# Optimization experiments

Measured on AMD Instinct MI355X. Metric: run time of the kernel, lower is better.

The kernel has to match this reference:

```python
import jax, jax.numpy as jnp
from jax import lax
import numpy as np

SEQ, BATCH, X_DIM = 256, 64, 64
FEAT = 256      # dense_x[-1]
DEC = 256       # dense_h_x[-1]
H = 512         # dim_rnn


def setup_inputs() -> dict:
    key = jax.random.key(0)
    ks = jax.random.split(key, 12)
    s = 0.05
    return {
        "x": jax.random.normal(ks[0], (SEQ, BATCH, X_DIM), jnp.float32),
        "mode_selector": jax.random.uniform(ks[1], (SEQ,), jnp.float32),
        # feature extractor: Linear(x_dim -> FEAT) + tanh
        "W_fx": jax.random.normal(ks[2], (FEAT, X_DIM), jnp.float32) * s,
        "b_fx": jnp.zeros((FEAT,), jnp.float32),
        # LSTM (single layer): gates ordered i, f, g, o (torch convention)
        "W_ih": jax.random.normal(ks[3], (4 * H, FEAT), jnp.float32) * s,
        "W_hh": jax.random.normal(ks[4], (4 * H, H), jnp.float32) * s,
        "b_ih": jnp.zeros((4 * H,), jnp.float32),
        "b_hh": jnp.zeros((4 * H,), jnp.float32),
        # decoder MLP: Linear(H -> DEC) + tanh
        "W_hx": jax.random.normal(ks[5], (DEC, H), jnp.float32) * s,
        "b_hx": jnp.zeros((DEC,), jnp.float32),
        # gen_out: Linear(DEC -> x_dim)
        "W_out": jax.random.normal(ks[6], (X_DIM, DEC), jnp.float32) * s,
        "b_out": jnp.zeros((X_DIM,), jnp.float32),
    }


def _forward(x, mode_selector, W_fx, b_fx, W_ih, W_hh, b_ih, b_hh,
             W_hx, b_hx, W_out, b_out):
    def fe(v):  # feature_extractor_x (dropout_p=0 -> identity)
        return jnp.tanh(v @ W_fx.T + b_fx)

    def gen(h):  # mlp_h_x + gen_out
        return jnp.tanh(h @ W_hx.T + b_hx) @ W_out.T + b_out

    def lstm_cell(feat, h, c):
        g = feat @ W_ih.T + b_ih + h @ W_hh.T + b_hh  # [B, 4H]
        i, f, gg, o = jnp.split(g, 4, axis=-1)
        c2 = jax.nn.sigmoid(f) * c + jax.nn.sigmoid(i) * jnp.tanh(gg)
        h2 = jax.nn.sigmoid(o) * jnp.tanh(c2)
        return h2, c2

    S, B, _ = x.shape
    feat_x = fe(x)  # [S, B, FEAT] teacher-forced features
    h0 = jnp.zeros((B, H), x.dtype)
    c0 = jnp.zeros((B, H), x.dtype)
    y0 = jnp.zeros((B, W_out.shape[0]), x.dtype)

    def step(carry, inp):
        h, c, y_prev = carry
        feat_tf, mix, is_first = inp
        # at t=0 original uses feature_x[0] as the "auto" feature
        feat_auto = jnp.where(is_first, feat_tf, fe(y_prev))
        feat = mix * feat_auto + (1.0 - mix) * feat_tf
        y_t = gen(h)           # generated from pre-update hidden state
        h2, c2 = lstm_cell(feat, h, c)
        return (h2, c2, y_t), y_t

    is_first = (jnp.arange(S) == 0)
    _, y = lax.scan(step, (h0, c0, y0), (feat_x, mode_selector, is_first))
    return y  # [S, B, x_dim]


def reference(x, mode_selector, W_fx, b_fx, W_ih, W_hh, b_ih, b_hh,
              W_hx, b_hx, W_out, b_out):
    return _forward(x, mode_selector, W_fx, b_fx, W_ih, W_hh, b_ih, b_hh,
                    W_hx, b_hx, W_out, b_out)
```

## Files before the change

kernel.cpp:

```cpp
#include <hip/hip_runtime.h>
#include <stdint.h>

typedef unsigned short u16;
typedef unsigned int u32;
typedef unsigned long long u64;
typedef __attribute__((ext_vector_type(8))) short short8;
typedef __attribute__((ext_vector_type(4))) float f32x4;
typedef __attribute__((ext_vector_type(4))) int int4v;

#define SEQ 256
#define GATE_WGS 64
#define D_WGS 8
#define NWG 73
#define A_ELE 49152
#define D_ELE 16384

__device__ __forceinline__ u16 f2bf(float f) {
  u32 u = __float_as_uint(f);
  u += 0x7FFFu + ((u >> 16) & 1u);
  return (u16)(u >> 16);
}
__device__ __forceinline__ float bf2f(u16 v) {
  return __uint_as_float(((u32)v) << 16);
}
__device__ __forceinline__ short8 cvt8(const float* __restrict__ p) {
  short8 r;
#pragma unroll
  for (int j = 0; j < 8; ++j) r[j] = (short)f2bf(p[j]);
  return r;
}
__device__ __forceinline__ short8 cvt8v(const float* __restrict__ p) {
  f32x4 a = *(const f32x4*)p, b = *(const f32x4*)(p + 4);
  short8 r;
#pragma unroll
  for (int j = 0; j < 4; ++j) { r[j] = (short)f2bf(a[j]); r[4 + j] = (short)f2bf(b[j]); }
  return r;
}
__device__ __forceinline__ float fast_tanh(float x) {
  return 1.0f - 2.0f / (1.0f + __expf(2.0f * x));
}
__device__ __forceinline__ float fast_sig(float x) {
  return 1.0f / (1.0f + __expf(-x));
}

union V16 { short8 s; u64 q[2]; };
__device__ __forceinline__ short8 ldc16(const u16* p) {
  V16 v;
  v.q[0] = __hip_atomic_load((const u64*)p,     __ATOMIC_RELAXED, __HIP_MEMORY_SCOPE_AGENT);
  v.q[1] = __hip_atomic_load((const u64*)p + 1, __ATOMIC_RELAXED, __HIP_MEMORY_SCOPE_AGENT);
  return v.s;
}
__device__ __forceinline__ void stc16(u16* p, const u64* s) {
  __hip_atomic_store((u64*)p,     s[0], __ATOMIC_RELAXED, __HIP_MEMORY_SCOPE_AGENT);
  __hip_atomic_store((u64*)p + 1, s[1], __ATOMIC_RELAXED, __HIP_MEMORY_SCOPE_AGENT);
}
__device__ __forceinline__ void pollge(u32* p, u32 v) {
  while (__hip_atomic_load(p, __ATOMIC_RELAXED, __HIP_MEMORY_SCOPE_AGENT) < v) {}
}
__device__ __forceinline__ void setflag(u32* p, u32 v) {
  __hip_atomic_store(p, v, __ATOMIC_RELAXED, __HIP_MEMORY_SCOPE_AGENT);
}
#define VMCNT0() asm volatile("s_waitcnt vmcnt(0)" ::: "memory")

__global__ void prep_misc(const float* __restrict__ W_fx, const float* __restrict__ b_fx,
                          const float* __restrict__ W_out, const float* __restrict__ b_out,
                          u16* __restrict__ Abuf0, u32* __restrict__ flags,
                          float* __restrict__ bcomb, u16* __restrict__ Wcpack) {
  int b = blockIdx.x, tid = threadIdx.x;
  if (b == 0) {
    for (int it = 0; it < 16; ++it) {
      int chunk = it * 256 + tid;
      *(int4v*)(Abuf0 + (2048 + chunk) * 8) = (int4v){0, 0, 0, 0};
    }
  } else if (b == 1) {
    for (int k = 0; k < 6; ++k) flags[k * 256 + tid] = 0u;
  } else if (b == 2) {
    float s = b_fx[tid];
    for (int k = 0; k < 64; ++k) s += W_fx[tid * 64 + k] * b_out[k];
    bcomb[tid] = s;
  } else {
    int ct = b - 3;
    for (int it = 0; it < 16; ++it) {
      int o = it * 256 + tid;
      int cl = o >> 8, dec = o & 255;
      int c = ct * 16 + cl;
      float s = 0.f;
      for (int k = 0; k < 64; ++k) s += W_fx[c * 64 + k] * W_out[k * 256 + dec];
      int dwk = dec >> 5, kd = dec & 31;
      int l = (c & 15) + ((kd >> 3) << 4), j = kd & 7;
      Wcpack[((dwk * 16 + (c >> 4)) * 64 + l) * 8 + j] = f2bf(s);
    }
  }
}

__global__ void prep_ftf(const float* __restrict__ x, const float* __restrict__ W_fx,
                         const float* __restrict__ b_fx, u16* __restrict__ ftf) {
  __shared__ __attribute__((aligned(16))) u16 fstage[64 * 264];
  const int t = blockIdx.x, tid = threadIdx.x;
  const int wv = tid >> 6, ln = tid & 63;
  const int c15 = ln & 15, qq = ln >> 4;
  short8 WfR[2][4];
#pragma unroll
  for (int kk = 0; kk < 2; ++kk)
#pragma unroll
    for (int nt = 0; nt < 4; ++nt)
      WfR[kk][nt] = cvt8(W_fx + ((wv * 4 + nt) * 16 + c15) * 64 + kk * 32 + qq * 8);
  float bfx_r[4];
#pragma unroll
  for (int nt = 0; nt < 4; ++nt) bfx_r[nt] = b_fx[(wv * 4 + nt) * 16 + c15];
  short8 xa[2][4];
#pragma unroll
  for (int kb = 0; kb < 2; ++kb)
#pragma unroll
    for (int mt = 0; mt < 4; ++mt)
      xa[kb][mt] = cvt8v(x + (t * 64 + mt * 16 + c15) * 64 + kb * 32 + qq * 8);
  f32x4 tf[4][4];
#pragma unroll
  for (int nt = 0; nt < 4; ++nt)
#pragma unroll
    for (int mt = 0; mt < 4; ++mt) tf[nt][mt] = (f32x4){0.f, 0.f, 0.f, 0.f};
#pragma unroll
  for (int kb = 0; kb < 2; ++kb)
#pragma unroll
    for (int nt = 0; nt < 4; ++nt)
#pragma unroll
      for (int mt = 0; mt < 4; ++mt)
        tf[nt][mt] = __builtin_amdgcn_mfma_f32_16x16x32_bf16(xa[kb][mt], WfR[kb][nt], tf[nt][mt], 0, 0, 0);
#pragma unroll
  for (int nt = 0; nt < 4; ++nt)
#pragma unroll
    for (int mt = 0; mt < 4; ++mt)
#pragma unroll
      for (int r2 = 0; r2 < 4; ++r2) {
        int row = mt * 16 + qq * 4 + r2;
        fstage[row * 264 + (wv * 4 + nt) * 16 + c15] = f2bf(fast_tanh(tf[nt][mt][r2] + bfx_r[nt]));
      }
  __syncthreads();
  u16* ftfb = ftf + t * 16384;
#pragma unroll
  for (int it = 0; it < 8; ++it) {
    int chunk = it * 256 + tid;
    int kb = chunk >> 8, l = chunk & 63;
    int m = ((chunk >> 6) & 3) * 16 + (l & 15);
    int k = kb * 32 + (l >> 4) * 8;
    *(short8*)(ftfb + chunk * 8) = *(const short8*)(fstage + m * 264 + k);
  }
}

__global__ void __launch_bounds__(256, 1)
rnn_kernel(const float* __restrict__ x, const float* __restrict__ msel,
           const float* __restrict__ W_ih, const float* __restrict__ W_hh,
           const float* __restrict__ b_ih, const float* __restrict__ b_hh,
           const float* __restrict__ W_hx, const float* __restrict__ b_hx,
           const float* __restrict__ W_out, const float* __restrict__ b_out,
           float* __restrict__ out,
           u16* __restrict__ Abase, u16* __restrict__ dbase,
           u32* __restrict__ flags,
           const float* __restrict__ bcomb, const u16* __restrict__ Wcpack,
           const u16* __restrict__ ftf, u16* __restrict__ fblend) {
  __shared__ __attribute__((aligned(16))) char smem[109568];
  const int wgid = blockIdx.x;
  const int tid = threadIdx.x;
  const int wv = tid >> 6, ln = tid & 63;
  u32* hcnt  = flags + 1168;
  u32* dcnt  = flags + 1232;
  u32* fbcnt = flags + 1296;

  if (wgid < GATE_WGS) {
    const int wg = wgid;
    float* red = (float*)smem;
    u16* hstage = (u16*)(smem + 32768);
    short8 Breg[6][2];
#pragma unroll
    for (int kk = 0; kk < 6; ++kk) {
      int kb = wv + kk * 4;
#pragma unroll
      for (int nt = 0; nt < 2; ++nt) {
        int n = ln & 15, q = ln >> 4;
        int gate = nt * 2 + (n >> 3), unit = n & 7;
        int row = gate * 512 + wg * 8 + unit;
        int k = kb * 32 + q * 8;
        const float* src = (k < 256) ? (W_ih + row * 256 + k) : (W_hh + row * 512 + (k - 256));
        Breg[kk][nt] = cvt8(src);
      }
    }
    float bsum_r[2][4];
#pragma unroll
    for (int it = 0; it < 2; ++it) {
      int u = (it * 256 + tid) & 7;
#pragma unroll
      for (int g = 0; g < 4; ++g) {
        int row = g * 512 + wg * 8 + u;
        bsum_r[it][g] = b_ih[row] + b_hh[row];
      }
    }
    float creg[2] = {0.f, 0.f};
    const int kbW = 8 + (wg >> 2), qW = wg & 3;
    int r = 0, rn = 1;
    for (int t = 0; t < SEQ; ++t) {
      if (tid < 4) pollge(&hcnt[tid * 16], (u32)(16 * t));
      else if (tid == 64 && t > 0)
        pollge(&fbcnt[(t & 1) * 16], 8u * ((u32)(t + 1) >> 1));
      __syncthreads();
      const u16* A = Abase + r * A_ELE;
      u16* An = Abase + rn * A_ELE;
      short8 a[6][4];
#pragma unroll
      for (int kk = 2; kk < 6; ++kk) {
        int kb = wv + kk * 4;
#pragma unroll
        for (int mt = 0; mt < 4; ++mt)
          a[kk][mt] = ldc16(A + ((kb * 4 + mt) * 64 + ln) * 8);
      }
      {
        const u16* fsrc = (t == 0) ? ftf : (fblend + (t & 1) * 16384);
#pragma unroll
        for (int kk = 0; kk < 2; ++kk) {
          int kb = wv + kk * 4;
#pragma unroll
          for (int mt = 0; mt < 4; ++mt)
            a[kk][mt] = ldc16(fsrc + ((kb * 4 + mt) * 64 + ln) * 8);
        }
      }
      f32x4 acc[2][4];
#pragma unroll
      for (int nt = 0; nt < 2; nt++)
#pragma unroll
        for (int mt = 0; mt < 4; mt++) acc[nt][mt] = (f32x4){0.f, 0.f, 0.f, 0.f};
#pragma unroll
      for (int kk = 0; kk < 6; ++kk)
#pragma unroll
        for (int nt = 0; nt < 2; nt++)
#pragma unroll
          for (int mt = 0; mt < 4; mt++)
            acc[nt][mt] = __builtin_amdgcn_mfma_f32_16x16x32_bf16(a[kk][mt], Breg[kk][nt], acc[nt][mt], 0, 0, 0);
#pragma unroll
      for (int nt = 0; nt < 2; nt++)
#pragma unroll
        for (int mt = 0; mt < 4; mt++)
          *(f32x4*)(red + ((wv * 8 + nt * 4 + mt) * 64 + ln) * 4) = acc[nt][mt];
      __syncthreads();
#pragma unroll
      for (int it = 0; it < 2; ++it) {
        int item = it * 256 + tid;
        int m = item >> 3, u = item & 7;
        int mt = m >> 4, lq = ((m & 15) >> 2) * 16, reg = m & 3;
        float g4[4];
#pragma unroll
        for (int g = 0; g < 4; ++g) {
          float s = bsum_r[it][g];
          int base = ((g >> 1) * 4 + mt) * 64 + lq + (g & 1) * 8 + u;
#pragma unroll
          for (int w = 0; w < 4; ++w) s += red[(w * 8 * 64 + base) * 4 + reg];
          g4[g] = s;
        }
        float ii = fast_sig(g4[0]), ff = fast_sig(g4[1]);
        float gg = fast_tanh(g4[2]), oo = fast_sig(g4[3]);
        float cn = ff * creg[it] + ii * gg;
        creg[it] = cn;
        float h = oo * fast_tanh(cn);
        hstage[(mt * 16 + (m & 15)) * 8 + u] = f2bf(h);
      }
      __syncthreads();
      if (tid < 64) {
        int mt2 = tid >> 4, m15 = tid & 15;
        u16* dst = An + (((kbW * 4 + mt2) * 64 + qW * 16 + m15) * 8);
        stc16(dst, (const u64*)(hstage + tid * 8));
        VMCNT0();
        if (tid == 0)
          (void)__hip_atomic_fetch_add(&hcnt[(wg & 3) * 16], 1u,
                                       __ATOMIC_RELAXED, __HIP_MEMORY_SCOPE_AGENT);
      }
      r = rn; rn = (rn == 2) ? 0 : rn + 1;
    }
  } else if (wgid < GATE_WGS + D_WGS) {
    const int dw = wgid - GATE_WGS;
    float* red = (float*)smem;
    u16* dstage = (u16*)(smem + 32768);
    float* fstg = (float*)(smem + 36864);
    short8 Breg[4][2];
#pragma unroll
    for (int kk = 0; kk < 4; ++kk) {
      int kbh = wv * 4 + kk;
#pragma unroll
      for (int nt = 0; nt < 2; ++nt) {
        int n = ln & 15, q = ln >> 4;
        int row = dw * 32 + nt * 16 + n;
        int k = kbh * 32 + q * 8;
        Breg[kk][nt] = cvt8(W_hx + row * 512 + k);
      }
    }
    short8 WcB[8][2];
#pragma unroll
    for (int kb = 0; kb < 8; ++kb)
#pragma unroll
      for (int ntl = 0; ntl < 2; ++ntl)
        WcB[kb][ntl] = *(const short8*)(Wcpack + ((kb * 16 + dw * 2 + ntl) * 64 + ln) * 8);
    float bias_r[8];
#pragma unroll
    for (int it = 0; it < 8; ++it) bias_r[it] = b_hx[dw * 32 + ((it * 256 + tid) & 31)];
    const int ci = dw * 256 + tid;
    const int m_bl = ((tid >> 6) & 3) * 16 + (tid & 15);
    const int cl0 = ((tid & 63) >> 4) * 8;
    f32x4 bc0 = *(const f32x4*)(bcomb + dw * 32 + cl0);
    f32x4 bc1 = *(const f32x4*)(bcomb + dw * 32 + cl0 + 4);
    int r = 0, rn = 1;
    for (int t = 0; t < SEQ; ++t) {
      if (tid < 4) pollge(&hcnt[tid * 16], (u32)(16 * t));
      __syncthreads();
      const u16* A = Abase + r * A_ELE;
      u16* dbufR = dbase + (t & 3) * D_ELE;
      short8 a[4][4];
#pragma unroll
      for (int kk = 0; kk < 4; ++kk)
#pragma unroll
        for (int mt = 0; mt < 4; ++mt)
          a[kk][mt] = ldc16(A + (((8 + wv * 4 + kk) * 4 + mt) * 64 + ln) * 8);
      f32x4 acc[2][4];
#pragma unroll
      for (int nt = 0; nt < 2; nt++)
#pragma unroll
        for (int mt = 0; mt < 4; mt++) acc[nt][mt] = (f32x4){0.f, 0.f, 0.f, 0.f};
#pragma unroll
      for (int kk = 0; kk < 4; ++kk)
#pragma unroll
        for (int nt = 0; nt < 2; nt++)
#pragma unroll
          for (int mt = 0; mt < 4; mt++)
            acc[nt][mt] = __builtin_amdgcn_mfma_f32_16x16x32_bf16(a[kk][mt], Breg[kk][nt], acc[nt][mt], 0, 0, 0);
#pragma unroll
      for (int nt = 0; nt < 2; nt++)
#pragma unroll
        for (int mt = 0; mt < 4; mt++)
          *(f32x4*)(red + ((wv * 8 + nt * 4 + mt) * 64 + ln) * 4) = acc[nt][mt];
      __syncthreads();
#pragma unroll
      for (int it = 0; it < 8; ++it) {
        int item = it * 256 + tid;
        int m = item >> 5, c = item & 31;
        int mt = m >> 4, lq = ((m & 15) >> 2) * 16, reg = m & 3;
        float s = bias_r[it];
        int base = ((c >> 4) * 4 + mt) * 64 + lq + (c & 15);
#pragma unroll
        for (int w = 0; w < 4; ++w) s += red[(w * 8 * 64 + base) * 4 + reg];
        dstage[((mt * 4 + (c >> 3)) * 16 + (m & 15)) * 8 + (c & 7)] = f2bf(fast_tanh(s));
      }
      __syncthreads();
      stc16(dbufR + (dw * 256 + tid) * 8, (const u64*)(dstage + tid * 8));
      VMCNT0();
      __syncthreads();
      if (tid == 0)
        (void)__hip_atomic_fetch_add(dcnt, 1u, __ATOMIC_RELAXED, __HIP_MEMORY_SCOPE_AGENT);
      if (t < SEQ - 1) {
        if (tid == 0) pollge(dcnt, 8u * (u32)(t + 1));
        __syncthreads();
        f32x4 pacc[2][4];
#pragma unroll
        for (int ntl = 0; ntl < 2; ++ntl)
#pragma unroll
          for (int mt = 0; mt < 4; ++mt) pacc[ntl][mt] = (f32x4){0.f, 0.f, 0.f, 0.f};
#pragma unroll
        for (int half = 0; half < 2; ++half) {
          short8 a2[4][4];
#pragma unroll
          for (int k2 = 0; k2 < 4; ++k2)
#pragma unroll
            for (int mt = 0; mt < 4; ++mt)
              a2[k2][mt] = ldc16(dbufR + (((half * 4 + k2) * 4 + mt) * 64 + ln) * 8);
#pragma unroll
          for (int k2 = 0; k2 < 4; ++k2)
#pragma unroll
            for (int ntl = 0; ntl < 2; ++ntl)
#pragma unroll
              for (int mt = 0; mt < 4; ++mt)
                pacc[ntl][mt] = __builtin_amdgcn_mfma_f32_16x16x32_bf16(a2[k2][mt], WcB[half * 4 + k2][ntl], pacc[ntl][mt], 0, 0, 0);
        }
#pragma unroll
        for (int ntl = 0; ntl < 2; ++ntl)
#pragma unroll
          for (int mt = 0; mt < 4; ++mt)
#pragma unroll
            for (int reg = 0; reg < 4; ++reg) {
              int m = mt * 16 + (ln >> 4) * 4 + reg;
              int cl = ntl * 16 + (ln & 15);
              fstg[m * 32 + cl] = pacc[ntl][mt][reg];
            }
        __syncthreads();
        float mixg = msel[t + 1];
        short8 tfv = *(const short8*)(ftf + (t + 1) * 16384 + ci * 8);
        short8 rr;
#pragma unroll
        for (int j = 0; j < 8; ++j) {
          float av = fstg[m_bl * 32 + cl0 + j] + ((j < 4) ? bc0[j] : bc1[j - 4]);
          float fv = mixg * fast_tanh(av) + (1.f - mixg) * bf2f((u16)tfv[j]);
          rr[j] = (short)f2bf(fv);
        }
        V16 v; v.s = rr;
        stc16(fblend + ((t + 1) & 1) * 16384 + ci * 8, v.q);
        VMCNT0();
        __syncthreads();
        if (tid == 0)
          (void)__hip_atomic_fetch_add(&fbcnt[((t + 1) & 1) * 16], 1u,
                                       __ATOMIC_RELAXED, __HIP_MEMORY_SCOPE_AGENT);
      }
      r = rn; rn = (rn == 2) ? 0 : rn + 1;
    }
  } else {
    float* red = (float*)smem;
    const int c15 = ln & 15, qq = ln >> 4;
    short8 WoR[2][4];
#pragma unroll
    for (int kk = 0; kk < 2; ++kk) {
      int koffo = (wv * 2 + kk) * 32 + qq * 8;
#pragma unroll
      for (int nt = 0; nt < 4; ++nt)
        WoR[kk][nt] = cvt8(W_out + (nt * 16 + c15) * 256 + koffo);
    }
    float bout_r = b_out[wv * 16 + c15];
    for (int t = 0; t < SEQ; ++t) {
      if (tid == 0) pollge(dcnt, 8u * (u32)(t + 1));
      __syncthreads();
      const u16* dbufR = dbase + (t & 3) * D_ELE;
      short8 da[2][4];
#pragma unroll
      for (int kk = 0; kk < 2; ++kk)
#pragma unroll
        for (int mt = 0; mt < 4; ++mt)
          da[kk][mt] = ldc16(dbufR + (((wv * 2 + kk) * 4 + mt) * 64 + ln) * 8);
      f32x4 acc[4][4];
#pragma unroll
      for (int nt = 0; nt < 4; nt++)
#pragma unroll
        for (int mt = 0; mt < 4; mt++) acc[nt][mt] = (f32x4){0.f, 0.f, 0.f, 0.f};
#pragma unroll
      for (int kk = 0; kk < 2; ++kk)
#pragma unroll
        for (int nt = 0; nt < 4; nt++)
#pragma unroll
          for (int mt = 0; mt < 4; mt++)
            acc[nt][mt] = __builtin_amdgcn_mfma_f32_16x16x32_bf16(da[kk][mt], WoR[kk][nt], acc[nt][mt], 0, 0, 0);
#pragma unroll
      for (int nt = 0; nt < 4; nt++)
#pragma unroll
        for (int mt = 0; mt < 4; mt++)
          *(f32x4*)(red + ((wv * 16 + nt * 4 + mt) * 64 + ln) * 4) = acc[nt][mt];
      __syncthreads();
#pragma unroll
      for (int mt = 0; mt < 4; ++mt) {
        f32x4 s = (f32x4){0.f, 0.f, 0.f, 0.f};
#pragma unroll
        for (int w2 = 0; w2 < 4; ++w2)
          s += *(const f32x4*)(red + ((w2 * 16 + wv * 4 + mt) * 64 + ln) * 4);
#pragma unroll
        for (int r2 = 0; r2 < 4; ++r2) {
          int row = mt * 16 + qq * 4 + r2;
          out[t * 4096 + row * 64 + wv * 16 + c15] = s[r2] + bout_r;
        }
      }
      __syncthreads();
    }
  }
}

extern "C" void kernel_launch(void* const* d_in, const int* in_sizes, int n_in,
                              void* d_out, int out_size, void* d_ws, size_t ws_size,
                              hipStream_t stream) {
  const float* x     = (const float*)d_in[0];
  const float* msel  = (const float*)d_in[1];
  const float* W_fx  = (const float*)d_in[2];
  const float* b_fx  = (const float*)d_in[3];
  const float* W_ih  = (const float*)d_in[4];
  const float* W_hh  = (const float*)d_in[5];
  const float* b_ih  = (const float*)d_in[6];
  const float* b_hh  = (const float*)d_in[7];
  const float* W_hx  = (const float*)d_in[8];
  const float* b_hx  = (const float*)d_in[9];
  const float* W_out = (const float*)d_in[10];
  const float* b_out = (const float*)d_in[11];

  uint8_t* ws = (uint8_t*)d_ws;
  u16*   Abase  = (u16*)ws;
  u16*   dbase  = (u16*)(ws + 294912);
  u32*   flags  = (u32*)(ws + 425984);
  float* bcomb  = (float*)(ws + 432128);
  u16*   Wcpack = (u16*)(ws + 433152);
  u16*   fblend = (u16*)(ws + 564224);
  u16*   ftf    = (u16*)(ws + 629760);

  prep_misc<<<19, 256, 0, stream>>>(W_fx, b_fx, W_out, b_out,
                                    Abase, flags, bcomb, Wcpack);
  prep_ftf<<<256, 256, 0, stream>>>(x, W_fx, b_fx, ftf);
  rnn_kernel<<<NWG, 256, 0, stream>>>(x, msel, W_ih, W_hh, b_ih, b_hh,
                                      W_hx, b_hx, W_out, b_out,
                                      (float*)d_out, Abase, dbase, flags,
                                      bcomb, Wcpack, ftf, fblend);
}
```

Baseline: 2.270 ms.

## Split decoder work by batch rows to drop inter-decoder barrier and overlap gate loads

The decoder workgroups now each own a 16-row batch slice (4 WGs instead of 8), computing the full W_hx output and the fused feedback features locally from LDS. This removes the second cross-workgroup wait on dcnt before the feedback GEMM. W_hx is pre-packed to bf16 in a prep kernel and streamed from global/L2 each step. Gate workgroups now start the hidden-state MFMAs before polling for the blended features, overlapping that wait with compute. The tradeoff is fewer decoder WGs doing more work each and more weight traffic per step.

```diff
diff --git a/kernel.cpp b/kernel.cpp
--- a/kernel.cpp
+++ b/kernel.cpp
@@ -10,8 +10,8 @@
 
 #define SEQ 256
 #define GATE_WGS 64
-#define D_WGS 8
-#define NWG 73
+#define D_WGS 4
+#define NWG 69
 #define A_ELE 49152
 #define D_ELE 16384
 
@@ -57,15 +57,14 @@
 __device__ __forceinline__ void pollge(u32* p, u32 v) {
   while (__hip_atomic_load(p, __ATOMIC_RELAXED, __HIP_MEMORY_SCOPE_AGENT) < v) {}
 }
-__device__ __forceinline__ void setflag(u32* p, u32 v) {
-  __hip_atomic_store(p, v, __ATOMIC_RELAXED, __HIP_MEMORY_SCOPE_AGENT);
-}
 #define VMCNT0() asm volatile("s_waitcnt vmcnt(0)" ::: "memory")
 
 __global__ void prep_misc(const float* __restrict__ W_fx, const float* __restrict__ b_fx,
                           const float* __restrict__ W_out, const float* __restrict__ b_out,
+                          const float* __restrict__ W_hx,
                           u16* __restrict__ Abuf0, u32* __restrict__ flags,
-                          float* __restrict__ bcomb, u16* __restrict__ Wcpack) {
+                          float* __restrict__ bcomb, u16* __restrict__ Wcpack,
+                          u16* __restrict__ Whx_pack) {
   int b = blockIdx.x, tid = threadIdx.x;
   if (b == 0) {
     for (int it = 0; it < 16; ++it) {
@@ -78,7 +77,7 @@
     float s = b_fx[tid];
     for (int k = 0; k < 64; ++k) s += W_fx[tid * 64 + k] * b_out[k];
     bcomb[tid] = s;
-  } else {
+  } else if (b < 19) {
     int ct = b - 3;
     for (int it = 0; it < 16; ++it) {
       int o = it * 256 + tid;
@@ -90,6 +89,16 @@
       int l = (c & 15) + ((kd >> 3) << 4), j = kd & 7;
       Wcpack[((dwk * 16 + (c >> 4)) * 64 + l) * 8 + j] = f2bf(s);
     }
+  } else {
+    int base = (b - 19) * 2048;
+#pragma unroll
+    for (int it = 0; it < 8; ++it) {
+      int cid = base + it * 256 + tid;
+      int kb = cid >> 10, rem = cid & 1023, nt16 = rem >> 6, l = rem & 63;
+      int row = nt16 * 16 + (l & 15);
+      int k = kb * 32 + ((l >> 4) << 3);
+      *(short8*)(Whx_pack + cid * 8) = cvt8v(W_hx + row * 512 + k);
+    }
   }
 }
 
@@ -151,12 +160,13 @@
 rnn_kernel(const float* __restrict__ x, const float* __restrict__ msel,
            const float* __restrict__ W_ih, const float* __restrict__ W_hh,
            const float* __restrict__ b_ih, const float* __restrict__ b_hh,
-           const float* __restrict__ W_hx, const float* __restrict__ b_hx,
+           const float* __restrict__ b_hx,
            const float* __restrict__ W_out, const float* __restrict__ b_out,
            float* __restrict__ out,
            u16* __restrict__ Abase, u16* __restrict__ dbase,
            u32* __restrict__ flags,
            const float* __restrict__ bcomb, const u16* __restrict__ Wcpack,
+           const u16* __restrict__ Whx_pack,
            const u16* __restrict__ ftf, u16* __restrict__ fblend) {
   __shared__ __attribute__((aligned(16))) char smem[109568];
   const int wgid = blockIdx.x;
@@ -199,41 +209,47 @@
     int r = 0, rn = 1;
     for (int t = 0; t < SEQ; ++t) {
       if (tid < 4) pollge(&hcnt[tid * 16], (u32)(16 * t));
-      else if (tid == 64 && t > 0)
-        pollge(&fbcnt[(t & 1) * 16], 8u * ((u32)(t + 1) >> 1));
       __syncthreads();
       const u16* A = Abase + r * A_ELE;
       u16* An = Abase + rn * A_ELE;
-      short8 a[6][4];
+      f32x4 acc[2][4];
+#pragma unroll
+      for (int nt = 0; nt < 2; nt++)
+#pragma unroll
+        for (int mt = 0; mt < 4; mt++) acc[nt][mt] = (f32x4){0.f, 0.f, 0.f, 0.f};
+      short8 ah[4][4];
 #pragma unroll
       for (int kk = 2; kk < 6; ++kk) {
         int kb = wv + kk * 4;
 #pragma unroll
         for (int mt = 0; mt < 4; ++mt)
-          a[kk][mt] = ldc16(A + ((kb * 4 + mt) * 64 + ln) * 8);
-      }
+          ah[kk - 2][mt] = ldc16(A + ((kb * 4 + mt) * 64 + ln) * 8);
+      }
+#pragma unroll
+      for (int kk = 2; kk < 6; ++kk)
+#pragma unroll
+        for (int nt = 0; nt < 2; nt++)
+#pragma unroll
+          for (int mt = 0; mt < 4; mt++)
+            acc[nt][mt] = __builtin_amdgcn_mfma_f32_16x16x32_bf16(ah[kk - 2][mt], Breg[kk][nt], acc[nt][mt], 0, 0, 0);
+      if (tid == 64 && t > 0) pollge(&fbcnt[(t & 1) * 16], 4u * ((u32)(t + 1) >> 1));
+      __syncthreads();
       {
         const u16* fsrc = (t == 0) ? ftf : (fblend + (t & 1) * 16384);
 #pragma unroll
         for (int kk = 0; kk < 2; ++kk) {
           int kb = wv + kk * 4;
+          short8 af[4];
 #pragma unroll
           for (int mt = 0; mt < 4; ++mt)
-            a[kk][mt] = ldc16(fsrc + ((kb * 4 + mt) * 64 + ln) * 8);
-        }
-      }
-      f32x4 acc[2][4];
-#pragma unroll
-      for (int nt = 0; nt < 2; nt++)
-#pragma unroll
-        for (int mt = 0; mt < 4; mt++) acc[nt][mt] = (f32x4){0.f, 0.f, 0.f, 0.f};
-#pragma unroll
-      for (int kk = 0; kk < 6; ++kk)
-#pragma unroll
-        for (int nt = 0; nt < 2; nt++)
-#pragma unroll
-          for (int mt = 0; mt < 4; mt++)
-            acc[nt][mt] = __builtin_amdgcn_mfma_f32_16x16x32_bf16(a[kk][mt], Breg[kk][nt], acc[nt][mt], 0, 0, 0);
+            af[mt] = ldc16(fsrc + ((kb * 4 + mt) * 64 + ln) * 8);
+#pragma unroll
+          for (int nt = 0; nt < 2; nt++)
+#pragma unroll
+            for (int mt = 0; mt < 4; mt++)
+              acc[nt][mt] = __builtin_amdgcn_mfma_f32_16x16x32_bf16(af[mt], Breg[kk][nt], acc[nt][mt], 0, 0, 0);
+        }
+      }
 #pragma unroll
       for (int nt = 0; nt < 2; nt++)
 #pragma unroll
@@ -275,133 +291,96 @@
     }
   } else if (wgid < GATE_WGS + D_WGS) {
     const int dw = wgid - GATE_WGS;
-    float* red = (float*)smem;
-    u16* dstage = (u16*)(smem + 32768);
-    float* fstg = (float*)(smem + 36864);
-    short8 Breg[4][2];
-#pragma unroll
-    for (int kk = 0; kk < 4; ++kk) {
-      int kbh = wv * 4 + kk;
-#pragma unroll
-      for (int nt = 0; nt < 2; ++nt) {
-        int n = ln & 15, q = ln >> 4;
-        int row = dw * 32 + nt * 16 + n;
-        int k = kbh * 32 + q * 8;
-        Breg[kk][nt] = cvt8(W_hx + row * 512 + k);
-      }
-    }
-    short8 WcB[8][2];
-#pragma unroll
-    for (int kb = 0; kb < 8; ++kb)
-#pragma unroll
-      for (int ntl = 0; ntl < 2; ++ntl)
-        WcB[kb][ntl] = *(const short8*)(Wcpack + ((kb * 16 + dw * 2 + ntl) * 64 + ln) * 8);
-    float bias_r[8];
-#pragma unroll
-    for (int it = 0; it < 8; ++it) bias_r[it] = b_hx[dw * 32 + ((it * 256 + tid) & 31)];
-    const int ci = dw * 256 + tid;
-    const int m_bl = ((tid >> 6) & 3) * 16 + (tid & 15);
-    const int cl0 = ((tid & 63) >> 4) * 8;
-    f32x4 bc0 = *(const f32x4*)(bcomb + dw * 32 + cl0);
-    f32x4 bc1 = *(const f32x4*)(bcomb + dw * 32 + cl0 + 4);
+    u16* dstage = (u16*)smem;
+    float* fstg = (float*)(smem + 8448);
+    float bhx_r[4];
+#pragma unroll
+    for (int ntl = 0; ntl < 4; ++ntl) bhx_r[ntl] = b_hx[(wv * 4 + ntl) * 16 + (ln & 15)];
     int r = 0, rn = 1;
     for (int t = 0; t < SEQ; ++t) {
       if (tid < 4) pollge(&hcnt[tid * 16], (u32)(16 * t));
       __syncthreads();
       const u16* A = Abase + r * A_ELE;
       u16* dbufR = dbase + (t & 3) * D_ELE;
-      short8 a[4][4];
-#pragma unroll
-      for (int kk = 0; kk < 4; ++kk)
-#pragma unroll
-        for (int mt = 0; mt < 4; ++mt)
-          a[kk][mt] = ldc16(A + (((8 + wv * 4 + kk) * 4 + mt) * 64 + ln) * 8);
-      f32x4 acc[2][4];
-#pragma unroll
-      for (int nt = 0; nt < 2; nt++)
-#pragma unroll
-        for (int mt = 0; mt < 4; mt++) acc[nt][mt] = (f32x4){0.f, 0.f, 0.f, 0.f};
-#pragma unroll
-      for (int kk = 0; kk < 4; ++kk)
-#pragma unroll
-        for (int nt = 0; nt < 2; nt++)
-#pragma unroll
-          for (int mt = 0; mt < 4; mt++)
-            acc[nt][mt] = __builtin_amdgcn_mfma_f32_16x16x32_bf16(a[kk][mt], Breg[kk][nt], acc[nt][mt], 0, 0, 0);
-#pragma unroll
-      for (int nt = 0; nt < 2; nt++)
-#pragma unroll
-        for (int mt = 0; mt < 4; mt++)
-          *(f32x4*)(red + ((wv * 8 + nt * 4 + mt) * 64 + ln) * 4) = acc[nt][mt];
-      __syncthreads();
-#pragma unroll
-      for (int it = 0; it < 8; ++it) {
-        int item = it * 256 + tid;
-        int m = item >> 5, c = item & 31;
-        int mt = m >> 4, lq = ((m & 15) >> 2) * 16, reg = m & 3;
-        float s = bias_r[it];
-        int base = ((c >> 4) * 4 + mt) * 64 + lq + (c & 15);
-#pragma unroll
-        for (int w = 0; w < 4; ++w) s += red[(w * 8 * 64 + base) * 4 + reg];
-        dstage[((mt * 4 + (c >> 3)) * 16 + (m & 15)) * 8 + (c & 7)] = f2bf(fast_tanh(s));
-      }
-      __syncthreads();
-      stc16(dbufR + (dw * 256 + tid) * 8, (const u64*)(dstage + tid * 8));
-      VMCNT0();
-      __syncthreads();
-      if (tid == 0)
-        (void)__hip_atomic_fetch_add(dcnt, 1u, __ATOMIC_RELAXED, __HIP_MEMORY_SCOPE_AGENT);
+      short8 ah[16];
+#pragma unroll
+      for (int kbh = 0; kbh < 16; ++kbh)
+        ah[kbh] = ldc16(A + (((8 + kbh) * 4 + dw) * 64 + ln) * 8);
+      f32x4 acc[4];
+#pragma unroll
+      for (int ntl = 0; ntl < 4; ++ntl) acc[ntl] = (f32x4){0.f, 0.f, 0.f, 0.f};
+#pragma unroll
+      for (int kbh = 0; kbh < 16; ++kbh) {
+#pragma unroll
+        for (int ntl = 0; ntl < 4; ++ntl) {
+          short8 bw = *(const short8*)(Whx_pack + ((kbh * 16 + wv * 4 + ntl) * 64 + ln) * 8);
+          acc[ntl] = __builtin_amdgcn_mfma_f32_16x16x32_bf16(ah[kbh], bw, acc[ntl], 0, 0, 0);
+        }
+      }
+#pragma unroll
+      for (int ntl = 0; ntl < 4; ++ntl)
+#pragma unroll
+        for (int reg = 0; reg < 4; ++reg)
+          dstage[((ln >> 4) * 4 + reg) * 264 + (wv * 4 + ntl) * 16 + (ln & 15)]
+              = f2bf(fast_tanh(acc[ntl][reg] + bhx_r[ntl]));
+      __syncthreads();
+#pragma unroll
+      for (int s = 0; s < 2; ++s) {
+        int cl = s * 256 + tid;
+        int kd = cl >> 6, l = cl & 63;
+        V16 v; v.s = *(const short8*)(dstage + (l & 15) * 264 + kd * 32 + (l >> 4) * 8);
+        stc16(dbufR + ((kd * 4 + dw) * 64 + l) * 8, v.q);
+      }
       if (t < SEQ - 1) {
-        if (tid == 0) pollge(dcnt, 8u * (u32)(t + 1));
-        __syncthreads();
-        f32x4 pacc[2][4];
-#pragma unroll
-        for (int ntl = 0; ntl < 2; ++ntl)
-#pragma unroll
-          for (int mt = 0; mt < 4; ++mt) pacc[ntl][mt] = (f32x4){0.f, 0.f, 0.f, 0.f};
-#pragma unroll
-        for (int half = 0; half < 2; ++half) {
-          short8 a2[4][4];
-#pragma unroll
-          for (int k2 = 0; k2 < 4; ++k2)
-#pragma unroll
-            for (int mt = 0; mt < 4; ++mt)
-              a2[k2][mt] = ldc16(dbufR + (((half * 4 + k2) * 4 + mt) * 64 + ln) * 8);
-#pragma unroll
-          for (int k2 = 0; k2 < 4; ++k2)
-#pragma unroll
-            for (int ntl = 0; ntl < 2; ++ntl)
-#pragma unroll
-              for (int mt = 0; mt < 4; ++mt)
-                pacc[ntl][mt] = __builtin_amdgcn_mfma_f32_16x16x32_bf16(a2[k2][mt], WcB[half * 4 + k2][ntl], pacc[ntl][mt], 0, 0, 0);
-        }
-#pragma unroll
-        for (int ntl = 0; ntl < 2; ++ntl)
-#pragma unroll
-          for (int mt = 0; mt < 4; ++mt)
-#pragma unroll
-            for (int reg = 0; reg < 4; ++reg) {
-              int m = mt * 16 + (ln >> 4) * 4 + reg;
-              int cl = ntl * 16 + (ln & 15);
-              fstg[m * 32 + cl] = pacc[ntl][mt][reg];
-            }
+        f32x4 acc2[4];
+#pragma unroll
+        for (int ntf = 0; ntf < 4; ++ntf) acc2[ntf] = (f32x4){0.f, 0.f, 0.f, 0.f};
+#pragma unroll
+        for (int kd = 0; kd < 8; ++kd) {
+          short8 ad = *(const short8*)(dstage + (ln & 15) * 264 + kd * 32 + (ln >> 4) * 8);
+#pragma unroll
+          for (int ntf = 0; ntf < 4; ++ntf) {
+            short8 bw = *(const short8*)(Wcpack + ((kd * 16 + wv * 4 + ntf) * 64 + ln) * 8);
+            acc2[ntf] = __builtin_amdgcn_mfma_f32_16x16x32_bf16(ad, bw, acc2[ntf], 0, 0, 0);
+          }
+        }
+#pragma unroll
+        for (int ntf = 0; ntf < 4; ++ntf)
+#pragma unroll
+          for (int reg = 0; reg < 4; ++reg)
+            fstg[((ln >> 4) * 4 + reg) * 264 + (wv * 4 + ntf) * 16 + (ln & 15)] = acc2[ntf][reg];
         __syncthreads();
         float mixg = msel[t + 1];
-        short8 tfv = *(const short8*)(ftf + (t + 1) * 16384 + ci * 8);
-        short8 rr;
-#pragma unroll
-        for (int j = 0; j < 8; ++j) {
-          float av = fstg[m_bl * 32 + cl0 + j] + ((j < 4) ? bc0[j] : bc1[j - 4]);
-          float fv = mixg * fast_tanh(av) + (1.f - mixg) * bf2f((u16)tfv[j]);
-          rr[j] = (short)f2bf(fv);
-        }
-        V16 v; v.s = rr;
-        stc16(fblend + ((t + 1) & 1) * 16384 + ci * 8, v.q);
+        const u16* ftfb = ftf + (t + 1) * 16384;
+        u16* fbl = fblend + ((t + 1) & 1) * 16384;
+#pragma unroll
+        for (int s = 0; s < 2; ++s) {
+          int cl = s * 256 + tid;
+          int kb = cl >> 6, l = cl & 63;
+          int c0 = kb * 32 + (l >> 4) * 8;
+          const float* fr = fstg + (l & 15) * 264 + c0;
+          short8 tfv = *(const short8*)(ftfb + ((kb * 4 + dw) * 64 + l) * 8);
+          short8 rr;
+#pragma unroll
+          for (int j = 0; j < 8; ++j) {
+            float av = fr[j] + bcomb[c0 + j];
+            rr[j] = (short)f2bf(mixg * fast_tanh(av) + (1.f - mixg) * bf2f((u16)tfv[j]));
+          }
+          V16 v; v.s = rr;
+          stc16(fbl + ((kb * 4 + dw) * 64 + l) * 8, v.q);
+        }
+        VMCNT0();
+        __syncthreads();
+        if (tid == 0) {
+          (void)__hip_atomic_fetch_add(dcnt, 1u, __ATOMIC_RELAXED, __HIP_MEMORY_SCOPE_AGENT);
+          (void)__hip_atomic_fetch_add(&fbcnt[((t + 1) & 1) * 16], 1u,
+                                       __ATOMIC_RELAXED, __HIP_MEMORY_SCOPE_AGENT);
+        }
+      } else {
         VMCNT0();
         __syncthreads();
         if (tid == 0)
-          (void)__hip_atomic_fetch_add(&fbcnt[((t + 1) & 1) * 16], 1u,
-                                       __ATOMIC_RELAXED, __HIP_MEMORY_SCOPE_AGENT);
+          (void)__hip_atomic_fetch_add(dcnt, 1u, __ATOMIC_RELAXED, __HIP_MEMORY_SCOPE_AGENT);
       }
       r = rn; rn = (rn == 2) ? 0 : rn + 1;
     }
@@ -418,7 +397,7 @@
     }
     float bout_r = b_out[wv * 16 + c15];
     for (int t = 0; t < SEQ; ++t) {
-      if (tid == 0) pollge(dcnt, 8u * (u32)(t + 1));
+      if (tid == 0) pollge(dcnt, 4u * (u32)(t + 1));
       __syncthreads();
       const u16* dbufR = dbase + (t & 3) * D_ELE;
       short8 da[2][4];
@@ -479,19 +458,20 @@
   const float* b_out = (const float*)d_in[11];
 
   uint8_t* ws = (uint8_t*)d_ws;
-  u16*   Abase  = (u16*)ws;
-  u16*   dbase  = (u16*)(ws + 294912);
-  u32*   flags  = (u32*)(ws + 425984);
-  float* bcomb  = (float*)(ws + 432128);
-  u16*   Wcpack = (u16*)(ws + 433152);
-  u16*   fblend = (u16*)(ws + 564224);
-  u16*   ftf    = (u16*)(ws + 629760);
-
-  prep_misc<<<19, 256, 0, stream>>>(W_fx, b_fx, W_out, b_out,
-                                    Abase, flags, bcomb, Wcpack);
+  u16*   Abase    = (u16*)ws;
+  u16*   dbase    = (u16*)(ws + 294912);
+  u32*   flags    = (u32*)(ws + 425984);
+  float* bcomb    = (float*)(ws + 432128);
+  u16*   Wcpack   = (u16*)(ws + 433152);
+  u16*   fblend   = (u16*)(ws + 564224);
+  u16*   Whx_pack = (u16*)(ws + 629760);
+  u16*   ftf      = (u16*)(ws + 891904);
+
+  prep_misc<<<27, 256, 0, stream>>>(W_fx, b_fx, W_out, b_out, W_hx,
+                                    Abase, flags, bcomb, Wcpack, Whx_pack);
   prep_ftf<<<256, 256, 0, stream>>>(x, W_fx, b_fx, ftf);
   rnn_kernel<<<NWG, 256, 0, stream>>>(x, msel, W_ih, W_hh, b_ih, b_hh,
-                                      W_hx, b_hx, W_out, b_out,
+                                      b_hx, W_out, b_out,
                                       (float*)d_out, Abase, dbase, flags,
-                                      bcomb, Wcpack, ftf, fblend);
-}
+                                      bcomb, Wcpack, Whx_pack, ftf, fblend);
+}
```

Result: no change. 2.299 ms (+1.3%).
